# Performance work log

Measured on AMD Instinct MI355X. Metric: run time of the kernel, lower is better.

The kernel has to match this reference:

```python
import jax, jax.numpy as jnp
import numpy as np

N_NODES = 50000
N_EDGES = 800000
N_GRAPHS = 256
D = 256
L = 3
BN_EPS = 1e-5


def setup_inputs() -> dict:
    key = jax.random.key(0)
    ks = jax.random.split(key, 8)
    x = jax.random.normal(ks[0], (N_NODES, D), dtype=jnp.float32)
    edge_index = jax.random.randint(ks[1], (2, N_EDGES), 0, N_NODES, dtype=jnp.int64)
    batch = jnp.sort(jax.random.randint(ks[2], (N_NODES,), 0, N_GRAPHS, dtype=jnp.int64))
    # small init scale keeps ReLU/BN chain numerically tame
    w1 = jax.random.normal(ks[3], (L, D, D), dtype=jnp.float32) * 0.05
    b1 = jnp.zeros((L, D), dtype=jnp.float32)
    w2 = jax.random.normal(ks[4], (L, D, D), dtype=jnp.float32) * 0.05
    b2 = jnp.zeros((L, D), dtype=jnp.float32)
    gamma = jnp.ones((L, D), dtype=jnp.float32)
    beta = jnp.zeros((L, D), dtype=jnp.float32)
    return {"x": x, "edge_index": edge_index, "batch": batch,
            "w1": w1, "b1": b1, "w2": w2, "b2": b2,
            "gamma": gamma, "beta": beta}


def reference(x, edge_index, batch, w1, b1, w2, b2, gamma, beta):
    src = edge_index[0]  # message senders (x_j)
    dst = edge_index[1]  # aggregation targets (x_i)
    h = x
    xs = []
    for i in range(L):
        # GINConv (eps=0): MLP(x_i + sum_{j in N(i)} x_j)
        agg = jax.ops.segment_sum(h[src], dst, num_segments=N_NODES)  # [N, D]
        z = h + agg
        z = jnp.maximum(z @ w1[i] + b1[i], 0.0) @ w2[i] + b2[i]  # Linear-ReLU-Linear
        z = jnp.maximum(z, 0.0)  # F.relu after conv
        # BatchNorm1d (training mode: biased batch stats over nodes)
        mean = jnp.mean(z, axis=0)
        var = jnp.var(z, axis=0)
        z = (z - mean) * jax.lax.rsqrt(var + BN_EPS) * gamma[i] + beta[i]
        xs.append(z)
        h = z
    # global_add_pool per layer, then concat along features -> [G, L*D]
    pooled = [jax.ops.segment_sum(xi, batch, num_segments=N_GRAPHS) for xi in xs]
    return jnp.concatenate(pooled, axis=1)
```

## Files before the change

kernel.cpp:

```cpp
#include <hip/hip_runtime.h>

#define NN 50000
#define NE 800000
#define NG 256
#define DD 256
#define NL 3
#define BN_EPS 1e-5f
#define MPAD 50048
#define CAP 96
#define MB2 782
#define NBIN 196
#define BINCAP 4608

typedef short bf16x8 __attribute__((ext_vector_type(8)));
typedef float f32x4 __attribute__((ext_vector_type(4)));
typedef unsigned short ushort8 __attribute__((ext_vector_type(8)));

__device__ __forceinline__ unsigned short f2bf(float f) {
    unsigned int u = __float_as_uint(f);
    u += 0x7FFFu + ((u >> 16) & 1u);
    return (unsigned short)(u >> 16);
}
__device__ __forceinline__ float bf2f(unsigned short s) {
    return __uint_as_float(((unsigned int)s) << 16);
}

#define R0 3200000
#define R1 393216
#define R2 12288
#define R3 256
#define R4 256
#define R5 NBIN
#define RTOT (R0 + R1 + R2 + R3 + R4 + R5)

__global__ void k_setup(const float* __restrict__ x, const float* __restrict__ w1,
                        const float* __restrict__ w2, const int* __restrict__ batch,
                        unsigned short* __restrict__ hbf, unsigned short* __restrict__ wt,
                        unsigned short* __restrict__ zbf, int* __restrict__ gstart,
                        int* __restrict__ bin_cnt) {
    int i = blockIdx.x * blockDim.x + threadIdx.x;
    if (i < R0) {
        float4 v = ((const float4*)x)[i];
        ushort4 o;
        o.x = f2bf(v.x); o.y = f2bf(v.y); o.z = f2bf(v.z); o.w = f2bf(v.w);
        ((ushort4*)hbf)[i] = o;
        return;
    }
    i -= R0;
    if (i < R1) {
        int mat = i >> 16;
        int n = (i >> 8) & 255;
        int k = i & 255;
        const float* src = (mat < 3) ? (w1 + ((size_t)mat << 16)) : (w2 + ((size_t)(mat - 3) << 16));
        wt[i] = f2bf(src[k * 256 + n]);
        return;
    }
    i -= R1;
    if (i < R2) { zbf[NN * DD + i] = 0; return; }
    i -= R2;
    if (i < R3) { hbf[(size_t)NN * DD + i] = 0; return; }
    i -= R3;
    if (i < R4) {
        int g = i;
        int lo = 0, hi = NN;
        while (lo < hi) {
            int mid = (lo + hi) >> 1;
            if (batch[mid] < g) lo = mid + 1; else hi = mid;
        }
        gstart[g] = lo;
        if (g == 0) gstart[NG] = NN;
        return;
    }
    i -= R4;
    if (i < R5) bin_cnt[i] = 0;
}

__global__ __launch_bounds__(256) void k_bin2(const int* __restrict__ ei,
                                              int* __restrict__ bin_cnt,
                                              unsigned int* __restrict__ binbuf) {
    __shared__ int hist[NBIN], base[NBIN], lcur[NBIN];
    int t = threadIdx.x;
    for (int i = t; i < NBIN; i += 256) { hist[i] = 0; lcur[i] = 0; }
    __syncthreads();
    int d[4], s[4];
    #pragma unroll
    for (int j = 0; j < 4; ++j) {
        int e = blockIdx.x * 1024 + j * 256 + t;
        if (e < NE) {
            s[j] = ei[e];
            d[j] = ei[NE + e];
            atomicAdd(&hist[d[j] >> 8], 1);
        } else d[j] = -1;
    }
    __syncthreads();
    for (int i = t; i < NBIN; i += 256)
        base[i] = hist[i] ? atomicAdd(&bin_cnt[i], hist[i]) : 0;
    __syncthreads();
    #pragma unroll
    for (int j = 0; j < 4; ++j) {
        if (d[j] >= 0) {
            int b = d[j] >> 8;
            int o = atomicAdd(&lcur[b], 1);
            binbuf[(size_t)b * BINCAP + base[b] + o] = (unsigned)s[j] | ((unsigned)(d[j] & 255) << 16);
        }
    }
}

__global__ __launch_bounds__(256) void k_bin3(const unsigned int* __restrict__ binbuf,
                                              const int* __restrict__ bin_cnt,
                                              unsigned short* __restrict__ elist,
                                              int* __restrict__ deg) {
    __shared__ int ldeg[256];
    int b = blockIdx.x, t = threadIdx.x;
    ldeg[t] = 0;
    __syncthreads();
    int cnt = bin_cnt[b];
    const unsigned int* bb = binbuf + (size_t)b * BINCAP;
    for (int i = t; i < cnt; i += 256) {
        unsigned v = bb[i];
        int src = v & 0xFFFF;
        int dl = v >> 16;
        int pos = atomicAdd(&ldeg[dl], 1);
        elist[(size_t)(b * 256 + dl) * CAP + pos] = (unsigned short)src;
    }
    __syncthreads();
    int node = b * 256 + t;
    if (node < NN) deg[node] = ldeg[t];
}

__global__ __launch_bounds__(256) void k_agg_bf(const unsigned short* __restrict__ h,
                                                const int* __restrict__ deg,
                                                const unsigned short* __restrict__ elist,
                                                unsigned short* __restrict__ z0) {
    int wave = threadIdx.x >> 6;
    int lane = threadIdx.x & 63;
    int node = blockIdx.x * 4 + wave;
    int chunk = lane & 31;
    int half = lane >> 5;
    const ushort8* h8 = (const ushort8*)h;

    float acc[8];
    if (half == 0) {
        ushort8 own = h8[(size_t)node * 32 + chunk];
        #pragma unroll
        for (int j = 0; j < 8; ++j) acc[j] = bf2f(own[j]);
    } else {
        #pragma unroll
        for (int j = 0; j < 8; ++j) acc[j] = 0.f;
    }

    int n = deg[node];
    const unsigned short* el = elist + (size_t)node * CAP;
    int i = 0;
    for (; i + 8 <= n; i += 8) {
        ushort8 sv = *(const ushort8*)(el + i);
        int i0 = half ? sv[1] : sv[0];
        int i1 = half ? sv[3] : sv[2];
        int i2 = half ? sv[5] : sv[4];
        int i3 = half ? sv[7] : sv[6];
        ushort8 r0 = h8[(size_t)i0 * 32 + chunk];
        ushort8 r1 = h8[(size_t)i1 * 32 + chunk];
        ushort8 r2 = h8[(size_t)i2 * 32 + chunk];
        ushort8 r3 = h8[(size_t)i3 * 32 + chunk];
        #pragma unroll
        for (int j = 0; j < 8; ++j) acc[j] += bf2f(r0[j]);
        #pragma unroll
        for (int j = 0; j < 8; ++j) acc[j] += bf2f(r1[j]);
        #pragma unroll
        for (int j = 0; j < 8; ++j) acc[j] += bf2f(r2[j]);
        #pragma unroll
        for (int j = 0; j < 8; ++j) acc[j] += bf2f(r3[j]);
    }
    for (; i < n; i += 2) {
        int s0 = el[i];
        int s1 = (i + 1 < n) ? (int)el[i + 1] : NN;
        int idx = half ? s1 : s0;
        ushort8 r = h8[(size_t)idx * 32 + chunk];
        #pragma unroll
        for (int j = 0; j < 8; ++j) acc[j] += bf2f(r[j]);
    }

    ushort8 o;
    #pragma unroll
    for (int j = 0; j < 8; ++j) {
        float other = __shfl_xor(acc[j], 32);
        o[j] = f2bf(acc[j] + other);
    }
    if (half == 0) ((ushort8*)z0)[(size_t)node * 32 + chunk] = o;
}

__global__ __launch_bounds__(256, 2) void k_mlp(const unsigned short* __restrict__ A,
                                                const unsigned short* __restrict__ BT1,
                                                const unsigned short* __restrict__ BT2,
                                                const float* __restrict__ b1,
                                                const float* __restrict__ b2,
                                                unsigned short* __restrict__ Cout,
                                                float* __restrict__ pstat) {
    __shared__ short As[64 * 64];
    __shared__ short Bs[256 * 64];
    __shared__ short H1[64 * 256];
    __shared__ float spart[256][2];
    int tid = threadIdx.x;
    int lane = tid & 63;
    int wc = tid >> 6;
    long m0 = (long)blockIdx.x * 64;
    const int r = lane & 15, hi = lane >> 4;

    f32x4 acc[4][4];
    #pragma unroll
    for (int m = 0; m < 4; ++m)
        #pragma unroll
        for (int n = 0; n < 4; ++n)
            acc[m][n] = (f32x4){0.f, 0.f, 0.f, 0.f};

    for (int k0 = 0; k0 < DD; k0 += 64) {
        #pragma unroll
        for (int p = 0; p < 2; ++p) {
            int flat = p * 256 + tid;
            int row = flat >> 3, c8 = flat & 7;
            int slot = c8 ^ (row & 7);
            *(bf16x8*)(As + row * 64 + slot * 8) =
                *(const bf16x8*)(A + (m0 + row) * DD + k0 + c8 * 8);
        }
        #pragma unroll
        for (int p = 0; p < 8; ++p) {
            int flat = p * 256 + tid;
            int row = flat >> 3, c8 = flat & 7;
            int slot = c8 ^ (row & 7);
            *(bf16x8*)(Bs + row * 64 + slot * 8) =
                *(const bf16x8*)(BT1 + (long)row * DD + k0 + c8 * 8);
        }
        __syncthreads();
        bf16x8 af[4][2], bfr[4][2];
        #pragma unroll
        for (int m = 0; m < 4; ++m) {
            int row = m * 16 + r;
            #pragma unroll
            for (int kk = 0; kk < 2; ++kk) {
                int slot = (kk * 4 + hi) ^ (row & 7);
                af[m][kk] = *(const bf16x8*)(As + row * 64 + slot * 8);
            }
        }
        #pragma unroll
        for (int n = 0; n < 4; ++n) {
            int col = wc * 64 + n * 16 + r;
            #pragma unroll
            for (int kk = 0; kk < 2; ++kk) {
                int slot = (kk * 4 + hi) ^ (col & 7);
                bfr[n][kk] = *(const bf16x8*)(Bs + col * 64 + slot * 8);
            }
        }
        #pragma unroll
        for (int kk = 0; kk < 2; ++kk)
            #pragma unroll
            for (int m = 0; m < 4; ++m)
                #pragma unroll
                for (int n = 0; n < 4; ++n)
                    acc[m][n] = __builtin_amdgcn_mfma_f32_16x16x32_bf16(af[m][kk], bfr[n][kk], acc[m][n], 0, 0, 0);
        __syncthreads();
    }

    #pragma unroll
    for (int n = 0; n < 4; ++n) {
        int col = wc * 64 + n * 16 + r;
        float bv = b1[col];
        int g = col >> 3, j8 = col & 7;
        #pragma unroll
        for (int m = 0; m < 4; ++m) {
            #pragma unroll
            for (int j = 0; j < 4; ++j) {
                int row = m * 16 + hi * 4 + j;
                float v = acc[m][n][j] + bv;
                v = v > 0.f ? v : 0.f;
                H1[row * 256 + (g ^ (row & 7)) * 8 + j8] = (short)f2bf(v);
            }
        }
    }
    #pragma unroll
    for (int m = 0; m < 4; ++m)
        #pragma unroll
        for (int n = 0; n < 4; ++n)
            acc[m][n] = (f32x4){0.f, 0.f, 0.f, 0.f};
    __syncthreads();

    for (int k0 = 0; k0 < DD; k0 += 64) {
        #pragma unroll
        for (int p = 0; p < 8; ++p) {
            int flat = p * 256 + tid;
            int row = flat >> 3, c8 = flat & 7;
            int slot = c8 ^ (row & 7);
            *(bf16x8*)(Bs + row * 64 + slot * 8) =
                *(const bf16x8*)(BT2 + (long)row * DD + k0 + c8 * 8);
        }
        __syncthreads();
        bf16x8 af[4][2], bfr[4][2];
        #pragma unroll
        for (int m = 0; m < 4; ++m) {
            int row = m * 16 + r;
            #pragma unroll
            for (int kk = 0; kk < 2; ++kk) {
                int g = (k0 >> 3) + kk * 4 + hi;
                af[m][kk] = *(const bf16x8*)(H1 + row * 256 + (g ^ (row & 7)) * 8);
            }
        }
        #pragma unroll
        for (int n = 0; n < 4; ++n) {
            int col = wc * 64 + n * 16 + r;
            #pragma unroll
            for (int kk = 0; kk < 2; ++kk) {
                int slot = (kk * 4 + hi) ^ (col & 7);
                bfr[n][kk] = *(const bf16x8*)(Bs + col * 64 + slot * 8);
            }
        }
        #pragma unroll
        for (int kk = 0; kk < 2; ++kk)
            #pragma unroll
            for (int m = 0; m < 4; ++m)
                #pragma unroll
                for (int n = 0; n < 4; ++n)
                    acc[m][n] = __builtin_amdgcn_mfma_f32_16x16x32_bf16(af[m][kk], bfr[n][kk], acc[m][n], 0, 0, 0);
        __syncthreads();
    }

    #pragma unroll
    for (int n = 0; n < 4; ++n) {
        int col = wc * 64 + n * 16 + r;
        float bv = b2[col];
        float cs = 0.f, cs2 = 0.f;
        #pragma unroll
        for (int m = 0; m < 4; ++m) {
            #pragma unroll
            for (int j = 0; j < 4; ++j) {
                long grow = m0 + m * 16 + hi * 4 + j;
                float v = acc[m][n][j] + bv;
                v = v > 0.f ? v : 0.f;
                Cout[grow * DD + col] = f2bf(v);
                float vm = (grow < NN) ? v : 0.f;
                cs += vm; cs2 += vm * vm;
            }
        }
        cs  += __shfl_xor(cs, 16);  cs  += __shfl_xor(cs, 32);
        cs2 += __shfl_xor(cs2, 16); cs2 += __shfl_xor(cs2, 32);
        if (hi == 0) {
            spart[col][0] = cs;
            spart[col][1] = cs2;
        }
    }
    __syncthreads();
    pstat[(size_t)blockIdx.x * 512 + tid] = spart[tid][0];
    pstat[(size_t)blockIdx.x * 512 + 256 + tid] = spart[tid][1];
}

__global__ __launch_bounds__(256) void k_bnscale2(const float* __restrict__ pstat,
                                                  const float* __restrict__ gamma,
                                                  const float* __restrict__ beta,
                                                  float* __restrict__ ss) {
    int c = blockIdx.x;
    int t = threadIdx.x;
    float s = 0.f, s2 = 0.f;
    for (int mb = t; mb < MB2; mb += 256) {
        s  += pstat[(size_t)mb * 512 + c];
        s2 += pstat[(size_t)mb * 512 + 256 + c];
    }
    __shared__ float rs[256], rs2[256];
    rs[t] = s; rs2[t] = s2;
    __syncthreads();
    #pragma unroll
    for (int d = 128; d > 0; d >>= 1) {
        if (t < d) { rs[t] += rs[t + d]; rs2[t] += rs2[t + d]; }
        __syncthreads();
    }
    if (t == 0) {
        float mean = rs[0] * (1.0f / NN);
        float var = rs2[0] * (1.0f / NN) - mean * mean;
        float sc = gamma[c] * rsqrtf(var + BN_EPS);
        ss[c] = sc;
        ss[DD + c] = beta[c] - mean * sc;
    }
}

template<int LAST>
__global__ __launch_bounds__(512) void k_bnpool(const unsigned short* __restrict__ z,
                                                const float* __restrict__ ss,
                                                const int* __restrict__ gstart,
                                                unsigned short* __restrict__ hbf,
                                                float* __restrict__ out, int layer) {
    __shared__ float4 red[16][32];
    int g = blockIdx.x;
    int ch = blockIdx.y;
    int t = threadIdx.x;
    int q = t & 31, rg = t >> 5;
    int cq = ch * 32 + q;
    float4 sc = ((const float4*)ss)[cq];
    float4 sh = ((const float4*)(ss + DD))[cq];
    int lo = gstart[g], hi = gstart[g + 1];
    float4 s = {0.f, 0.f, 0.f, 0.f};
    const ushort4* z4 = (const ushort4*)z;
    ushort4* h4 = (ushort4*)hbf;
    for (int r = lo + rg; r < hi; r += 16) {
        ushort4 zv = z4[(size_t)r * 64 + cq];
        float4 v;
        v.x = bf2f(zv.x) * sc.x + sh.x;
        v.y = bf2f(zv.y) * sc.y + sh.y;
        v.z = bf2f(zv.z) * sc.z + sh.z;
        v.w = bf2f(zv.w) * sc.w + sh.w;
        s.x += v.x; s.y += v.y; s.z += v.z; s.w += v.w;
        if (!LAST) {
            ushort4 o;
            o.x = f2bf(v.x); o.y = f2bf(v.y); o.z = f2bf(v.z); o.w = f2bf(v.w);
            h4[(size_t)r * 64 + cq] = o;
        }
    }
    red[rg][q] = s;
    __syncthreads();
    #pragma unroll
    for (int d = 8; d > 0; d >>= 1) {
        if (rg < d) {
            float4 a = red[rg][q], b = red[rg + d][q];
            a.x += b.x; a.y += b.y; a.z += b.z; a.w += b.w;
            red[rg][q] = a;
        }
        __syncthreads();
    }
    if (rg == 0) {
        ((float4*)(out + (size_t)g * (NL * DD) + layer * DD))[cq] = red[0][q];
    }
}

extern "C" void kernel_launch(void* const* d_in, const int* in_sizes, int n_in,
                              void* d_out, int out_size, void* d_ws, size_t ws_size,
                              hipStream_t stream) {
    const float* x     = (const float*)d_in[0];
    const int*   ei    = (const int*)d_in[1];
    const int*   batch = (const int*)d_in[2];
    const float* w1    = (const float*)d_in[3];
    const float* b1    = (const float*)d_in[4];
    const float* w2    = (const float*)d_in[5];
    const float* b2    = (const float*)d_in[6];
    const float* gamma = (const float*)d_in[7];
    const float* beta  = (const float*)d_in[8];
    float* out = (float*)d_out;

    char* ws = (char*)d_ws;
    size_t off = 0;
    auto alloc = [&](size_t bytes) -> void* {
        void* p = ws + off;
        off += (bytes + 255) & ~size_t(255);
        return p;
    };
    unsigned short* zB   = (unsigned short*)alloc((size_t)MPAD * DD * 2);
    unsigned short* zbf  = (unsigned short*)alloc((size_t)MPAD * DD * 2);
    unsigned short* hbf  = (unsigned short*)alloc((size_t)(NN + 64) * DD * 2);
    unsigned short* wt   = (unsigned short*)alloc((size_t)6 * DD * DD * 2);
    int* deg    = (int*)alloc((size_t)NN * 4);
    unsigned short* elist = (unsigned short*)alloc((size_t)NN * CAP * 2);
    unsigned int* binbuf = (unsigned int*)alloc((size_t)NBIN * BINCAP * 4);
    int* bin_cnt    = (int*)alloc(NBIN * 4);
    int* gstart = (int*)alloc((size_t)(NG + 1) * 4);
    float* pstat = (float*)alloc((size_t)MB2 * 512 * 4);
    float* ss   = (float*)alloc(2 * DD * 4);

    k_setup<<<(RTOT + 255) / 256, 256, 0, stream>>>(x, w1, w2, batch, hbf, wt, zbf, gstart, bin_cnt);
    const int EB = (NE + 1023) / 1024;
    k_bin2<<<EB, 256, 0, stream>>>(ei, bin_cnt, binbuf);
    k_bin3<<<NBIN, 256, 0, stream>>>(binbuf, bin_cnt, elist, deg);

    for (int l = 0; l < NL; ++l) {
        k_agg_bf<<<NN / 4, 256, 0, stream>>>(hbf, deg, elist, zbf);
        k_mlp<<<MB2, 256, 0, stream>>>(zbf, wt + (size_t)l * DD * DD,
                                       wt + (size_t)(3 + l) * DD * DD,
                                       b1 + l * DD, b2 + l * DD, zB, pstat);
        k_bnscale2<<<DD, 256, 0, stream>>>(pstat, gamma + l * DD, beta + l * DD, ss);
        if (l < NL - 1)
            k_bnpool<0><<<dim3(NG, 2), 512, 0, stream>>>(zB, ss, gstart, hbf, out, l);
        else
            k_bnpool<1><<<dim3(NG, 2), 512, 0, stream>>>(zB, ss, gstart, hbf, out, l);
    }
}
```

Baseline: 361.4 us.

## Fuse neighbor aggregation into MLP kernel, gathering rows directly into LDS

Removes the separate aggregation kernel and instead has each MLP block gather its 64 nodes' neighbor sums straight into shared memory, reusing that buffer for the hidden activations. This eliminates the intermediate bf16 global buffer write/read and a launch per layer. The trade-off is that the latency-bound gather now runs with far fewer waves in flight (782 blocks, occupancy limited by LDS and launch bounds), reducing memory-level parallelism.

Result: slower. 507.4 us (+40.4%).

```diff
diff --git a/kernel.cpp b/kernel.cpp
--- a/kernel.cpp
+++ b/kernel.cpp
@@ -27,17 +27,15 @@
 
 #define R0 3200000
 #define R1 393216
-#define R2 12288
+#define R2 256
 #define R3 256
-#define R4 256
-#define R5 NBIN
-#define RTOT (R0 + R1 + R2 + R3 + R4 + R5)
+#define R4 NBIN
+#define RTOT (R0 + R1 + R2 + R3 + R4)
 
 __global__ void k_setup(const float* __restrict__ x, const float* __restrict__ w1,
                         const float* __restrict__ w2, const int* __restrict__ batch,
                         unsigned short* __restrict__ hbf, unsigned short* __restrict__ wt,
-                        unsigned short* __restrict__ zbf, int* __restrict__ gstart,
-                        int* __restrict__ bin_cnt) {
+                        int* __restrict__ gstart, int* __restrict__ bin_cnt) {
     int i = blockIdx.x * blockDim.x + threadIdx.x;
     if (i < R0) {
         float4 v = ((const float4*)x)[i];
@@ -56,11 +54,9 @@
         return;
     }
     i -= R1;
-    if (i < R2) { zbf[NN * DD + i] = 0; return; }
+    if (i < R2) { hbf[(size_t)NN * DD + i] = 0; return; }
     i -= R2;
-    if (i < R3) { hbf[(size_t)NN * DD + i] = 0; return; }
-    i -= R3;
-    if (i < R4) {
+    if (i < R3) {
         int g = i;
         int lo = 0, hi = NN;
         while (lo < hi) {
@@ -71,8 +67,8 @@
         if (g == 0) gstart[NG] = NN;
         return;
     }
-    i -= R4;
-    if (i < R5) bin_cnt[i] = 0;
+    i -= R3;
+    if (i < R4) bin_cnt[i] = 0;
 }
 
 __global__ __launch_bounds__(256) void k_bin2(const int* __restrict__ ei,
@@ -128,84 +124,88 @@
     if (node < NN) deg[node] = ldeg[t];
 }
 
-__global__ __launch_bounds__(256) void k_agg_bf(const unsigned short* __restrict__ h,
+__global__ __launch_bounds__(256, 2) void k_mlp(const unsigned short* __restrict__ hbf,
                                                 const int* __restrict__ deg,
                                                 const unsigned short* __restrict__ elist,
-                                                unsigned short* __restrict__ z0) {
-    int wave = threadIdx.x >> 6;
-    int lane = threadIdx.x & 63;
-    int node = blockIdx.x * 4 + wave;
-    int chunk = lane & 31;
-    int half = lane >> 5;
-    const ushort8* h8 = (const ushort8*)h;
-
-    float acc[8];
-    if (half == 0) {
-        ushort8 own = h8[(size_t)node * 32 + chunk];
-        #pragma unroll
-        for (int j = 0; j < 8; ++j) acc[j] = bf2f(own[j]);
-    } else {
-        #pragma unroll
-        for (int j = 0; j < 8; ++j) acc[j] = 0.f;
-    }
-
-    int n = deg[node];
-    const unsigned short* el = elist + (size_t)node * CAP;
-    int i = 0;
-    for (; i + 8 <= n; i += 8) {
-        ushort8 sv = *(const ushort8*)(el + i);
-        int i0 = half ? sv[1] : sv[0];
-        int i1 = half ? sv[3] : sv[2];
-        int i2 = half ? sv[5] : sv[4];
-        int i3 = half ? sv[7] : sv[6];
-        ushort8 r0 = h8[(size_t)i0 * 32 + chunk];
-        ushort8 r1 = h8[(size_t)i1 * 32 + chunk];
-        ushort8 r2 = h8[(size_t)i2 * 32 + chunk];
-        ushort8 r3 = h8[(size_t)i3 * 32 + chunk];
-        #pragma unroll
-        for (int j = 0; j < 8; ++j) acc[j] += bf2f(r0[j]);
-        #pragma unroll
-        for (int j = 0; j < 8; ++j) acc[j] += bf2f(r1[j]);
-        #pragma unroll
-        for (int j = 0; j < 8; ++j) acc[j] += bf2f(r2[j]);
-        #pragma unroll
-        for (int j = 0; j < 8; ++j) acc[j] += bf2f(r3[j]);
-    }
-    for (; i < n; i += 2) {
-        int s0 = el[i];
-        int s1 = (i + 1 < n) ? (int)el[i + 1] : NN;
-        int idx = half ? s1 : s0;
-        ushort8 r = h8[(size_t)idx * 32 + chunk];
-        #pragma unroll
-        for (int j = 0; j < 8; ++j) acc[j] += bf2f(r[j]);
-    }
-
-    ushort8 o;
-    #pragma unroll
-    for (int j = 0; j < 8; ++j) {
-        float other = __shfl_xor(acc[j], 32);
-        o[j] = f2bf(acc[j] + other);
-    }
-    if (half == 0) ((ushort8*)z0)[(size_t)node * 32 + chunk] = o;
-}
-
-__global__ __launch_bounds__(256, 2) void k_mlp(const unsigned short* __restrict__ A,
                                                 const unsigned short* __restrict__ BT1,
                                                 const unsigned short* __restrict__ BT2,
                                                 const float* __restrict__ b1,
                                                 const float* __restrict__ b2,
                                                 unsigned short* __restrict__ Cout,
                                                 float* __restrict__ pstat) {
-    __shared__ short As[64 * 64];
+    __shared__ short ZH[64 * 256];
     __shared__ short Bs[256 * 64];
-    __shared__ short H1[64 * 256];
     __shared__ float spart[256][2];
     int tid = threadIdx.x;
     int lane = tid & 63;
-    int wc = tid >> 6;
+    int wv = tid >> 6;
     long m0 = (long)blockIdx.x * 64;
     const int r = lane & 15, hi = lane >> 4;
 
+    {
+        int chunk = lane & 31;
+        int half = lane >> 5;
+        const ushort8* h8 = (const ushort8*)hbf;
+        for (int p = 0; p < 16; ++p) {
+            int row = wv * 16 + p;
+            long node = m0 + row;
+            if (node < NN) {
+                float acc8[8];
+                if (half == 0) {
+                    ushort8 own = h8[(size_t)node * 32 + chunk];
+                    #pragma unroll
+                    for (int j = 0; j < 8; ++j) acc8[j] = bf2f(own[j]);
+                } else {
+                    #pragma unroll
+                    for (int j = 0; j < 8; ++j) acc8[j] = 0.f;
+                }
+                int n = deg[node];
+                const unsigned short* el = elist + (size_t)node * CAP;
+                int i = 0;
+                for (; i + 8 <= n; i += 8) {
+                    ushort8 sv = *(const ushort8*)(el + i);
+                    int i0 = half ? sv[1] : sv[0];
+                    int i1 = half ? sv[3] : sv[2];
+                    int i2 = half ? sv[5] : sv[4];
+                    int i3 = half ? sv[7] : sv[6];
+                    ushort8 r0 = h8[(size_t)i0 * 32 + chunk];
+                    ushort8 r1 = h8[(size_t)i1 * 32 + chunk];
+                    ushort8 r2 = h8[(size_t)i2 * 32 + chunk];
+                    ushort8 r3 = h8[(size_t)i3 * 32 + chunk];
+                    #pragma unroll
+                    for (int j = 0; j < 8; ++j) acc8[j] += bf2f(r0[j]);
+                    #pragma unroll
+                    for (int j = 0; j < 8; ++j) acc8[j] += bf2f(r1[j]);
+                    #pragma unroll
+                    for (int j = 0; j < 8; ++j) acc8[j] += bf2f(r2[j]);
+                    #pragma unroll
+                    for (int j = 0; j < 8; ++j) acc8[j] += bf2f(r3[j]);
+                }
+                for (; i < n; i += 2) {
+                    int s0 = el[i];
+                    int s1 = (i + 1 < n) ? (int)el[i + 1] : NN;
+                    int idx = half ? s1 : s0;
+                    ushort8 rr = h8[(size_t)idx * 32 + chunk];
+                    #pragma unroll
+                    for (int j = 0; j < 8; ++j) acc8[j] += bf2f(rr[j]);
+                }
+                ushort8 o;
+                #pragma unroll
+                for (int j = 0; j < 8; ++j) {
+                    float other = __shfl_xor(acc8[j], 32);
+                    o[j] = f2bf(acc8[j] + other);
+                }
+                if (half == 0)
+                    *(ushort8*)(ZH + row * 256 + ((chunk ^ (row & 7))) * 8) = o;
+            } else {
+                if (half == 0) {
+                    ushort8 o = (ushort8){0,0,0,0,0,0,0,0};
+                    *(ushort8*)(ZH + row * 256 + ((chunk ^ (row & 7))) * 8) = o;
+                }
+            }
+        }
+    }
+
     f32x4 acc[4][4];
     #pragma unroll
     for (int m = 0; m < 4; ++m)
@@ -214,14 +214,6 @@
             acc[m][n] = (f32x4){0.f, 0.f, 0.f, 0.f};
 
     for (int k0 = 0; k0 < DD; k0 += 64) {
-        #pragma unroll
-        for (int p = 0; p < 2; ++p) {
-            int flat = p * 256 + tid;
-            int row = flat >> 3, c8 = flat & 7;
-            int slot = c8 ^ (row & 7);
-            *(bf16x8*)(As + row * 64 + slot * 8) =
-                *(const bf16x8*)(A + (m0 + row) * DD + k0 + c8 * 8);
-        }
         #pragma unroll
         for (int p = 0; p < 8; ++p) {
             int flat = p * 256 + tid;
@@ -237,13 +229,13 @@
             int row = m * 16 + r;
             #pragma unroll
             for (int kk = 0; kk < 2; ++kk) {
-                int slot = (kk * 4 + hi) ^ (row & 7);
-                af[m][kk] = *(const bf16x8*)(As + row * 64 + slot * 8);
+                int g = (k0 >> 3) + kk * 4 + hi;
+                af[m][kk] = *(const bf16x8*)(ZH + row * 256 + (g ^ (row & 7)) * 8);
             }
         }
         #pragma unroll
         for (int n = 0; n < 4; ++n) {
-            int col = wc * 64 + n * 16 + r;
+            int col = wv * 64 + n * 16 + r;
             #pragma unroll
             for (int kk = 0; kk < 2; ++kk) {
                 int slot = (kk * 4 + hi) ^ (col & 7);
@@ -262,7 +254,7 @@
 
     #pragma unroll
     for (int n = 0; n < 4; ++n) {
-        int col = wc * 64 + n * 16 + r;
+        int col = wv * 64 + n * 16 + r;
         float bv = b1[col];
         int g = col >> 3, j8 = col & 7;
         #pragma unroll
@@ -272,7 +264,7 @@
                 int row = m * 16 + hi * 4 + j;
                 float v = acc[m][n][j] + bv;
                 v = v > 0.f ? v : 0.f;
-                H1[row * 256 + (g ^ (row & 7)) * 8 + j8] = (short)f2bf(v);
+                ZH[row * 256 + (g ^ (row & 7)) * 8 + j8] = (short)f2bf(v);
             }
         }
     }
@@ -300,12 +292,12 @@
             #pragma unroll
             for (int kk = 0; kk < 2; ++kk) {
                 int g = (k0 >> 3) + kk * 4 + hi;
-                af[m][kk] = *(const bf16x8*)(H1 + row * 256 + (g ^ (row & 7)) * 8);
+                af[m][kk] = *(const bf16x8*)(ZH + row * 256 + (g ^ (row & 7)) * 8);
             }
         }
         #pragma unroll
         for (int n = 0; n < 4; ++n) {
-            int col = wc * 64 + n * 16 + r;
+            int col = wv * 64 + n * 16 + r;
             #pragma unroll
             for (int kk = 0; kk < 2; ++kk) {
                 int slot = (kk * 4 + hi) ^ (col & 7);
@@ -324,7 +316,7 @@
 
     #pragma unroll
     for (int n = 0; n < 4; ++n) {
-        int col = wc * 64 + n * 16 + r;
+        int col = wv * 64 + n * 16 + r;
         float bv = b2[col];
         float cs = 0.f, cs2 = 0.f;
         #pragma unroll
@@ -449,7 +441,6 @@
         return p;
     };
     unsigned short* zB   = (unsigned short*)alloc((size_t)MPAD * DD * 2);
-    unsigned short* zbf  = (unsigned short*)alloc((size_t)MPAD * DD * 2);
     unsigned short* hbf  = (unsigned short*)alloc((size_t)(NN + 64) * DD * 2);
     unsigned short* wt   = (unsigned short*)alloc((size_t)6 * DD * DD * 2);
     int* deg    = (int*)alloc((size_t)NN * 4);
@@ -460,14 +451,14 @@
     float* pstat = (float*)alloc((size_t)MB2 * 512 * 4);
     float* ss   = (float*)alloc(2 * DD * 4);
 
-    k_setup<<<(RTOT + 255) / 256, 256, 0, stream>>>(x, w1, w2, batch, hbf, wt, zbf, gstart, bin_cnt);
+    k_setup<<<(RTOT + 255) / 256, 256, 0, stream>>>(x, w1, w2, batch, hbf, wt, gstart, bin_cnt);
     const int EB = (NE + 1023) / 1024;
     k_bin2<<<EB, 256, 0, stream>>>(ei, bin_cnt, binbuf);
     k_bin3<<<NBIN, 256, 0, stream>>>(binbuf, bin_cnt, elist, deg);
 
     for (int l = 0; l < NL; ++l) {
-        k_agg_bf<<<NN / 4, 256, 0, stream>>>(hbf, deg, elist, zbf);
-        k_mlp<<<MB2, 256, 0, stream>>>(zbf, wt + (size_t)l * DD * DD,
+        k_mlp<<<MB2, 256, 0, stream>>>(hbf, deg, elist,
+                                       wt + (size_t)l * DD * DD,
                                        wt + (size_t)(3 + l) * DD * DD,
                                        b1 + l * DD, b2 + l * DD, zB, pstat);
         k_bnscale2<<<DD, 256, 0, stream>>>(pstat, gamma + l * DD, beta + l * DD, ss);
```
